# Performance work log

Hardware: AMD Instinct MI355X
Metric: run time of the kernel (lower is better)

## Reference

```python
import jax, jax.numpy as jnp
import numpy as np

N_NODES, N_EDGES, F_IN, HID, PROJ, N_CLS, N_GRAPHS, T_EMB = 50000, 800000, 128, 128, 512, 32, 256, 768
EPS_BN, EPS_LN = 1e-5, 1e-5


def setup_inputs() -> dict:
    key = jax.random.key(0)
    ks = jax.random.split(key, 24)
    s = 0.05
    inp = {
        "x": jax.random.normal(ks[0], (N_NODES, F_IN), jnp.float32),
        "edge_index": jax.random.randint(ks[1], (2, N_EDGES), 0, N_NODES),
        "batch": jnp.sort(jax.random.randint(ks[2], (N_NODES,), 0, N_GRAPHS)),
        "text_feats": jax.random.normal(ks[3], (N_GRAPHS, T_EMB), jnp.float32),
        # 4 stacked GCN layers (all 128->128), each with BatchNorm affine params
        "gcn_W": jax.random.normal(ks[4], (4, F_IN, HID), jnp.float32) * s,
        "gcn_b": jnp.zeros((4, HID), jnp.float32),
        "bn_g": jnp.ones((4, HID), jnp.float32),
        "bn_b": jnp.zeros((4, HID), jnp.float32),
        # graph projection head
        "gpj_W1": jax.random.normal(ks[5], (HID, PROJ), jnp.float32) * s,
        "gpj_b1": jnp.zeros((PROJ,), jnp.float32),
        "gpj_W2": jax.random.normal(ks[6], (PROJ, PROJ), jnp.float32) * s,
        "gpj_b2": jnp.zeros((PROJ,), jnp.float32),
        "gpj_g": jnp.ones((PROJ,), jnp.float32),
        "gpj_be": jnp.zeros((PROJ,), jnp.float32),
        "gcl_W": jax.random.normal(ks[7], (PROJ, N_CLS), jnp.float32) * s,
        "gcl_b": jnp.zeros((N_CLS,), jnp.float32),
        # text projection head
        "tpj_W1": jax.random.normal(ks[8], (T_EMB, PROJ), jnp.float32) * s,
        "tpj_b1": jnp.zeros((PROJ,), jnp.float32),
        "tpj_W2": jax.random.normal(ks[9], (PROJ, PROJ), jnp.float32) * s,
        "tpj_b2": jnp.zeros((PROJ,), jnp.float32),
        "tpj_g": jnp.ones((PROJ,), jnp.float32),
        "tpj_be": jnp.zeros((PROJ,), jnp.float32),
        "tcl_W": jax.random.normal(ks[10], (PROJ, N_CLS), jnp.float32) * s,
        "tcl_b": jnp.zeros((N_CLS,), jnp.float32),
    }
    return inp


def _gcn_layer(x, src, dst, dnorm, W, b):
    # PyG GCNConv with self-loops and symmetric normalization
    xw = x @ W  # [N, H]
    coef = dnorm[src] * dnorm[dst]  # [E]
    agg = jax.ops.segment_sum(xw[src] * coef[:, None], dst, num_segments=N_NODES)
    agg = agg + xw * (dnorm * dnorm)[:, None]  # self-loop contribution
    return agg + b


def _batch_norm(x, g, b):
    mu = jnp.mean(x, axis=0)
    var = jnp.mean((x - mu) ** 2, axis=0)
    return (x - mu) * jax.lax.rsqrt(var + EPS_BN) * g + b


def _projection_head(x, W1, b1, W2, b2, g, be):
    projected = x @ W1 + b1
    h = jax.nn.gelu(projected, approximate=False)
    h = h @ W2 + b2
    h = h + projected  # residual (dropout in eval mode = identity)
    mu = jnp.mean(h, axis=-1, keepdims=True)
    var = jnp.mean((h - mu) ** 2, axis=-1, keepdims=True)
    return (h - mu) * jax.lax.rsqrt(var + EPS_LN) * g + be


def reference(x, edge_index, batch, text_feats, gcn_W, gcn_b, bn_g, bn_b,
              gpj_W1, gpj_b1, gpj_W2, gpj_b2, gpj_g, gpj_be, gcl_W, gcl_b,
              tpj_W1, tpj_b1, tpj_W2, tpj_b2, tpj_g, tpj_be, tcl_W, tcl_b):
    src, dst = edge_index[0], edge_index[1]
    deg = jax.ops.segment_sum(jnp.ones((N_EDGES,), x.dtype), dst, num_segments=N_NODES) + 1.0
    dnorm = jax.lax.rsqrt(deg)
    h = x
    for i in range(4):  # input block, 2 hidden blocks, output block
        h = _gcn_layer(h, src, dst, dnorm, gcn_W[i], gcn_b[i])
        h = jax.nn.leaky_relu(h, negative_slope=0.01)
        h = _batch_norm(h, bn_g[i], bn_b[i])
    # global mean pool over graphs
    sums = jax.ops.segment_sum(h, batch, num_segments=N_GRAPHS)
    cnts = jax.ops.segment_sum(jnp.ones((N_NODES,), h.dtype), batch, num_segments=N_GRAPHS)
    g_emb = sums / jnp.maximum(cnts, 1.0)[:, None]  # [G, HID]

    graph_proj = _projection_head(g_emb, gpj_W1, gpj_b1, gpj_W2, gpj_b2, gpj_g, gpj_be)
    graph_logp = jax.nn.log_softmax(graph_proj @ gcl_W + gcl_b, axis=-1)

    text_proj = _projection_head(text_feats, tpj_W1, tpj_b1, tpj_W2, tpj_b2, tpj_g, tpj_be)
    text_logp = jax.nn.log_softmax(text_proj @ tcl_W + tcl_b, axis=-1)

    return (graph_proj, text_proj, graph_logp, text_logp)
```

## Files before the change

### kernel.cpp

```cpp
#include <hip/hip_runtime.h>
#include <hip/hip_bf16.h>

#define N_NODES 50000
#define N_EDGES 800000
#define F_IN    128
#define HID     128
#define PROJ    512
#define N_CLS   32
#define N_GRAPHS 256
#define T_EMB   768
#define NB_SCAN ((N_NODES + 255) / 256)
#define DBINS   1024
#define NBROW   ((N_NODES + 63) / 64)
#define NBG2    ((NBROW + 1) / 2)
#define SHW     6250
#define ESLICE  ((N_EDGES + 4095) / 4096)

typedef __attribute__((ext_vector_type(8))) short bf16x8;
typedef __attribute__((ext_vector_type(4))) float f32x4;

__device__ __forceinline__ float bf2f(unsigned short u) {
    unsigned v = ((unsigned)u) << 16;
    return __uint_as_float(v);
}
__device__ __forceinline__ unsigned short f2us(float v) {
    __hip_bfloat16 b = __float2bfloat16(v);
    union { __hip_bfloat16 b; unsigned short u; } c; c.b = b; return c.u;
}

__global__ __launch_bounds__(256) void k_deg(const int* __restrict__ ei,
                                             int* __restrict__ cnt, int nE) {
    int bx = blockIdx.x;
    int s = bx & 7;
    int slice = bx >> 3;
    int lo = s * SHW, hi = lo + SHW;
    int base = slice * 4096 + threadIdx.x;
#pragma unroll 4
    for (int u = 0; u < 16; u++) {
        int e = base + u * 256;
        if (e < nE) {
            int d = ei[nE + e];
            if (d >= lo && d < hi) atomicAdd(cnt + d, 1);
        }
    }
}

__global__ __launch_bounds__(256) void k_scan1(const int* __restrict__ cnt,
    int* __restrict__ rowstart, float* __restrict__ dnorm, int* __restrict__ bsum)
{
    __shared__ int ps[256];
    int t = threadIdx.x;
    int i = blockIdx.x * 256 + t;
    int c = (i < N_NODES) ? cnt[i] : 0;
    if (i < N_NODES) dnorm[i] = rsqrtf((float)c + 1.0f);
    ps[t] = c;
    __syncthreads();
    for (int off = 1; off < 256; off <<= 1) {
        int v = (t >= off) ? ps[t - off] : 0;
        __syncthreads();
        ps[t] += v;
        __syncthreads();
    }
    if (i < N_NODES) rowstart[i] = ps[t] - c;
    if (t == 255) bsum[blockIdx.x] = ps[255];
}

__global__ __launch_bounds__(256) void k_scan2(int* __restrict__ bsum) {
    __shared__ int ps[256];
    int t = threadIdx.x;
    int v = (t < NB_SCAN) ? bsum[t] : 0;
    ps[t] = v;
    __syncthreads();
    for (int off = 1; off < 256; off <<= 1) {
        int u = (t >= off) ? ps[t - off] : 0;
        __syncthreads();
        ps[t] += u;
        __syncthreads();
    }
    if (t < NB_SCAN) bsum[t] = ps[t] - v;
}

__global__ __launch_bounds__(256) void k_scan3(int* __restrict__ rowstart,
    const int* __restrict__ bsum, const int* __restrict__ cnt,
    int* __restrict__ dhist)
{
    __shared__ int lh[DBINS];
    int t = threadIdx.x;
    for (int k = t; k < DBINS; k += 256) lh[k] = 0;
    __syncthreads();
    int i = blockIdx.x * 256 + t;
    if (i < N_NODES) {
        rowstart[i] += bsum[blockIdx.x];
        atomicAdd(&lh[min(cnt[i], DBINS - 1)], 1);
    }
    if (i == 0) rowstart[N_NODES] = N_EDGES;
    __syncthreads();
    for (int k = t; k < DBINS; k += 256) {
        int v = lh[k];
        if (v) atomicAdd(dhist + k, v);
    }
}

__global__ __launch_bounds__(256) void k_dscan(const int* __restrict__ dhist,
                                               int* __restrict__ doff) {
    __shared__ int part[256];
    __shared__ int binv[DBINS];
    int t = threadIdx.x;
    int base = t * 4;
    int g0 = dhist[DBINS - 1 - (base + 0)];
    int g1 = dhist[DBINS - 1 - (base + 1)];
    int g2 = dhist[DBINS - 1 - (base + 2)];
    int g3 = dhist[DBINS - 1 - (base + 3)];
    int s = g0 + g1 + g2 + g3;
    part[t] = s;
    __syncthreads();
    for (int off = 1; off < 256; off <<= 1) {
        int v = (t >= off) ? part[t - off] : 0;
        __syncthreads();
        part[t] += v;
        __syncthreads();
    }
    int run = part[t] - s;
    binv[base + 0] = run; run += g0;
    binv[base + 1] = run; run += g1;
    binv[base + 2] = run; run += g2;
    binv[base + 3] = run; run += g3;
    __syncthreads();
    for (int k = t; k < DBINS; k += 256) doff[DBINS - 1 - k] = binv[k];
}

__global__ __launch_bounds__(1024) void k_dperm(const int* __restrict__ cnt,
    int* __restrict__ doff, int* __restrict__ rowperm)
{
    __shared__ int lh[DBINS];
    __shared__ int lbase[DBINS];
    int t = threadIdx.x;
    if (t < DBINS) lh[t] = 0;
    __syncthreads();
    int i = blockIdx.x * 1024 + t;
    int bin = 0, lrank = 0;
    bool ok = i < N_NODES;
    if (ok) {
        bin = min(cnt[i], DBINS - 1);
        lrank = atomicAdd(&lh[bin], 1);
    }
    __syncthreads();
    if (t < DBINS) {
        int v = lh[t];
        if (v) lbase[t] = atomicAdd(doff + t, v);
    }
    __syncthreads();
    if (ok) rowperm[lbase[bin] + lrank] = i;
}

__global__ __launch_bounds__(256) void k_fill(const int* __restrict__ ei,
    const int* __restrict__ rowstart, int* __restrict__ cursor,
    int* __restrict__ srcl, int nE)
{
    int bx = blockIdx.x;
    int s = bx & 7;
    int slice = bx >> 3;
    int lo = s * SHW, hi = lo + SHW;
    int base = slice * 4096 + threadIdx.x;
#pragma unroll 4
    for (int u = 0; u < 16; u++) {
        int e = base + u * 256;
        if (e < nE) {
            int d = ei[nE + e];
            if (d >= lo && d < hi) {
                int pos = rowstart[d] + atomicAdd(cursor + d, 1);
                srcl[pos] = ei[e];
            }
        }
    }
}

__global__ void k_prep(const float* __restrict__ W, unsigned short* __restrict__ Wt,
                       const int* __restrict__ batch, int* __restrict__ gstart) {
    int t = blockIdx.x * 256 + threadIdx.x;
    if (t < 4 * 128 * 128) {
        int l = t >> 14;
        int k = (t >> 7) & 127;
        int n = t & 127;
        Wt[(size_t)l * 16384 + n * 128 + k] = f2us(W[(size_t)l * 16384 + k * 128 + n]);
    } else {
        int r = t - 4 * 128 * 128;
        if (r <= N_NODES) {
            int b  = (r < N_NODES) ? batch[r] : N_GRAPHS;
            int bp = (r > 0) ? batch[r - 1] : -1;
            for (int g = bp + 1; g <= b && g <= N_GRAPHS; g++) gstart[g] = r;
        }
    }
}

__global__ __launch_bounds__(256) void k_gcn_mm_mfma(const void* __restrict__ inp,
    const unsigned short* __restrict__ Wt,
    const float* __restrict__ stats, const float* __restrict__ bng,
    const float* __restrict__ bnb, const float* __restrict__ dnorm,
    unsigned short* __restrict__ ph, int n)
{
    __shared__ __align__(16) unsigned short Bs[128][136];
    __shared__ float scs[128], shs[128];
    int t = threadIdx.x;
    int row0 = blockIdx.x * 64;

    if (stats && t < 128) {
        float inv_n = 1.0f / (float)N_NODES;
        float mu = stats[t] * inv_n;
        float var = stats[128 + t] * inv_n - mu * mu;
        float rs = rsqrtf(var + 1e-5f);
        float sc = rs * bng[t];
        scs[t] = sc;
        shs[t] = bnb[t] - mu * sc;
    }
#pragma unroll
    for (int i = 0; i < 8; i++) {
        int c = t + i * 256;
        int nn = c >> 4;
        int k8 = (c & 15) * 8;
        *(uint4*)&Bs[nn][k8] = *(const uint4*)(Wt + (size_t)nn * 128 + k8);
    }
    __syncthreads();

    int w = t >> 6, lane = t & 63;
    int m = lane & 15, quad = lane >> 4;
    int arow = row0 + w * 16 + m;
    bool rowok = arow < n;

    bf16x8 afrag[4];
    if (!stats) {
        const float* inf = (const float*)inp;
#pragma unroll
        for (int ki = 0; ki < 4; ki++) {
            int k8 = ki * 32 + quad * 8;
            float4 v0 = make_float4(0.f, 0.f, 0.f, 0.f);
            float4 v1 = make_float4(0.f, 0.f, 0.f, 0.f);
            if (rowok) {
                v0 = *(const float4*)(inf + (size_t)arow * 128 + k8);
                v1 = *(const float4*)(inf + (size_t)arow * 128 + k8 + 4);
            }
            union { unsigned short u[8]; bf16x8 v; } pk;
            pk.u[0] = f2us(v0.x); pk.u[1] = f2us(v0.y); pk.u[2] = f2us(v0.z); pk.u[3] = f2us(v0.w);
            pk.u[4] = f2us(v1.x); pk.u[5] = f2us(v1.y); pk.u[6] = f2us(v1.z); pk.u[7] = f2us(v1.w);
            afrag[ki] = pk.v;
        }
    } else {
        const unsigned short* inb = (const unsigned short*)inp;
#pragma unroll
        for (int ki = 0; ki < 4; ki++) {
            int k8 = ki * 32 + quad * 8;
            uint4 raw = make_uint4(0, 0, 0, 0);
            if (rowok) raw = *(const uint4*)(inb + (size_t)arow * 128 + k8);
            unsigned rr[4] = { raw.x, raw.y, raw.z, raw.w };
            union { unsigned short u[8]; bf16x8 v; } pk;
#pragma unroll
            for (int j = 0; j < 4; j++) {
                int f0 = k8 + 2 * j, f1 = k8 + 2 * j + 1;
                float a0 = bf2f((unsigned short)rr[j]) * scs[f0] + shs[f0];
                float a1 = bf2f((unsigned short)(rr[j] >> 16)) * scs[f1] + shs[f1];
                pk.u[2 * j] = f2us(a0);
                pk.u[2 * j + 1] = f2us(a1);
            }
            afrag[ki] = pk.v;
        }
    }

    f32x4 acc[8];
#pragma unroll
    for (int nt = 0; nt < 8; nt++) acc[nt] = (f32x4){0.f, 0.f, 0.f, 0.f};
#pragma unroll
    for (int ki = 0; ki < 4; ki++) {
#pragma unroll
        for (int nt = 0; nt < 8; nt++) {
            bf16x8 b = *(const bf16x8*)&Bs[nt * 16 + m][ki * 32 + quad * 8];
            acc[nt] = __builtin_amdgcn_mfma_f32_16x16x32_bf16(afrag[ki], b, acc[nt], 0, 0, 0);
        }
    }

    float dn[4];
#pragma unroll
    for (int reg = 0; reg < 4; reg++) {
        int gr = row0 + w * 16 + quad * 4 + reg;
        dn[reg] = (gr < n) ? dnorm[gr] : 0.f;
    }

    __syncthreads();
#pragma unroll
    for (int nt = 0; nt < 8; nt++) {
#pragma unroll
        for (int reg = 0; reg < 4; reg++) {
            Bs[w * 16 + quad * 4 + reg][nt * 16 + m] = f2us(acc[nt][reg] * dn[reg]);
        }
    }
    __syncthreads();
#pragma unroll
    for (int i = 0; i < 4; i++) {
        int idx = t + i * 256;
        int r = idx >> 4;
        int c8 = (idx & 15) * 8;
        int gr = row0 + r;
        int ch = c8 >> 5;
        int off = c8 & 31;
        if (gr < n)
            *(uint4*)(ph + (size_t)ch * (N_NODES * 32) + (size_t)gr * 32 + off)
                = *(const uint4*)&Bs[r][c8];
    }
}

__global__ __launch_bounds__(256) void k_gather_c(const uint4* __restrict__ ph128,
    const int* __restrict__ srcl, const int* __restrict__ rowstart,
    const int* __restrict__ rowperm, const float* __restrict__ dnorm,
    const float* __restrict__ bias, unsigned short* __restrict__ outbb,
    float* __restrict__ stats, int n)
{
    const int EMAX = N_EDGES - 1;
    __shared__ float bsm[32], bqm[32];
    int t = threadIdx.x;
    if (t < 32) { bsm[t] = 0.f; bqm[t] = 0.f; }
    __syncthreads();

    int bx = blockIdx.x;
    int xcd = bx & 7;
    int c = xcd >> 1;
    int rb = (bx >> 3) * 2 + (xcd & 1);
    if (rb >= NBROW) return;
    int lane = t & 63;
    int w = t >> 6;
    int grp = lane >> 2;
    int l4 = lane & 3;
    int idx = rb * 64 + w * 16 + grp;
    bool rok = idx < n;
    int r = rok ? rowperm[idx] : 0;
    int start = rowstart[r];
    int deg = rowstart[r + 1] - start;
    float dnr = dnorm[r];
    if (!rok) { deg = 0; dnr = 0.f; }
    int len = deg + 1;

    const uint4* phc = ph128 + (size_t)c * (N_NODES * 4);

    float bi[8];
#pragma unroll
    for (int k = 0; k < 8; k++) bi[k] = bias[c * 32 + l4 * 8 + k];

    float a[8];
#pragma unroll
    for (int k = 0; k < 8; k++) a[k] = 0.f;

    for (int j = 0; j < len; j += 4) {
        uint4 uv[4];
#pragma unroll
        for (int u = 0; u < 4; u++) {
            int i = j + u;
            int sl = srcl[min(start + i, EMAX)];
            int s = (i < deg) ? sl : r;
            uv[u] = phc[(size_t)s * 4 + l4];
        }
#pragma unroll
        for (int u = 0; u < 4; u++) {
            int i = j + u;
            float wt = (i < len) ? 1.f : 0.f;
            unsigned rr[4] = { uv[u].x, uv[u].y, uv[u].z, uv[u].w };
#pragma unroll
            for (int d = 0; d < 4; d++) {
                a[2 * d]     += wt * bf2f((unsigned short)rr[d]);
                a[2 * d + 1] += wt * bf2f((unsigned short)(rr[d] >> 16));
            }
        }
    }

    float v[8];
#pragma unroll
    for (int k = 0; k < 8; k++) {
        float x = a[k] * dnr + bi[k];
        v[k] = x > 0.f ? x : 0.01f * x;
    }
    if (rok) {
        union { unsigned short us[8]; uint4 u; } ov;
#pragma unroll
        for (int k = 0; k < 8; k++) ov.us[k] = f2us(v[k]);
        *(uint4*)(outbb + (size_t)r * 128 + c * 32 + l4 * 8) = ov.u;
    } else {
#pragma unroll
        for (int k = 0; k < 8; k++) v[k] = 0.f;
    }

    float q[8];
#pragma unroll
    for (int k = 0; k < 8; k++) q[k] = v[k] * v[k];
#pragma unroll
    for (int mk = 4; mk < 64; mk <<= 1) {
#pragma unroll
        for (int k = 0; k < 8; k++) {
            v[k] += __shfl_xor(v[k], mk, 64);
            q[k] += __shfl_xor(q[k], mk, 64);
        }
    }
    if (grp == 0) {
#pragma unroll
        for (int k = 0; k < 8; k++) {
            atomicAdd(&bsm[l4 * 8 + k], v[k]);
            atomicAdd(&bqm[l4 * 8 + k], q[k]);
        }
    }
    __syncthreads();
    if (t < 32) {
        atomicAdd(&stats[c * 32 + t], bsm[t]);
        atomicAdd(&stats[128 + c * 32 + t], bqm[t]);
    }
}

__global__ __launch_bounds__(256) void k_pool2(const unsigned short* __restrict__ outbb,
    const int* __restrict__ gstart, const float* __restrict__ stats,
    const float* __restrict__ bng, const float* __restrict__ bnb,
    float* __restrict__ gemb)
{
    __shared__ float scs[128], shs[128];
    int g = blockIdx.x;
    int t = threadIdx.x;
    if (t < 128) {
        float inv_n = 1.0f / (float)N_NODES;
        float mu = stats[t] * inv_n;
        float var = stats[128 + t] * inv_n - mu * mu;
        float rs = rsqrtf(var + 1e-5f);
        float sc = rs * bng[t];
        scs[t] = sc;
        shs[t] = bnb[t] - mu * sc;
    }
    __syncthreads();
    int f = t & 127;
    int half = t >> 7;
    int start = gstart[g], end = gstart[g + 1];
    int cnt = end - start;
    float s0 = 0.f, s1 = 0.f, s2 = 0.f, s3 = 0.f;
    int r = start + half;
    for (; r + 6 < end; r += 8) {
        s0 += bf2f(outbb[(size_t)(r    ) * 128 + f]);
        s1 += bf2f(outbb[(size_t)(r + 2) * 128 + f]);
        s2 += bf2f(outbb[(size_t)(r + 4) * 128 + f]);
        s3 += bf2f(outbb[(size_t)(r + 6) * 128 + f]);
    }
    for (; r < end; r += 2) s0 += bf2f(outbb[(size_t)r * 128 + f]);
    float sum = (s0 + s1) + (s2 + s3);
    __shared__ float sb[256];
    sb[t] = sum;
    __syncthreads();
    if (t < 128) {
        float tot = sb[t] + sb[t + 128];
        float v = (cnt > 0) ? (tot / (float)cnt) * scs[f] + shs[f] : 0.f;
        gemb[(size_t)g * 128 + f] = v;
    }
}

__global__ __launch_bounds__(256) void k_head1x(const float* __restrict__ gemb,
    const float* __restrict__ textf,
    const float* __restrict__ gW1, const float* __restrict__ tW1,
    float* __restrict__ projg, float* __restrict__ projt6)
{
    __shared__ float ins[8][128];
    int bx = blockIdx.x;
    int kc = blockIdx.z;
    int isT = bx >= 32;
    if (!isT && kc > 0) return;
    int rb = isT ? bx - 32 : bx;
    const float* in = isT ? textf : gemb;
    int K = isT ? T_EMB : HID;
    const float* W = isT ? tW1 : gW1;
    float* outp = isT ? (projt6 + (size_t)kc * (N_GRAPHS * PROJ)) : projg;
    int k0 = kc * 128;

    int t = threadIdx.x;
    {
        int r = t >> 5, k = (t & 31) * 4;
        *(float4*)&ins[r][k] = *(const float4*)(in + (size_t)(rb * 8 + r) * K + k0 + k);
    }
    __syncthreads();
    int col = blockIdx.y * 128 + (t & 127);
    int rg = t >> 7;
    float acc[4] = { 0.f, 0.f, 0.f, 0.f };
    const float* Wp = W + (size_t)k0 * 512 + col;
#pragma unroll 8
    for (int k = 0; k < 128; k++) {
        float w = Wp[(size_t)k * 512];
#pragma unroll
        for (int i = 0; i < 4; i++) acc[i] += ins[rg * 4 + i][k] * w;
    }
#pragma unroll
    for (int i = 0; i < 4; i++) {
        int row = rb * 8 + rg * 4 + i;
        outp[(size_t)row * 512 + col] = acc[i];
    }
}

__global__ __launch_bounds__(256) void k_head2c(
    const float* __restrict__ projg, const float* __restrict__ projt6,
    const float* __restrict__ gb1, const float* __restrict__ tb1,
    const float* __restrict__ gW2, const float* __restrict__ gb2,
    const float* __restrict__ gg, const float* __restrict__ gbe,
    const float* __restrict__ gclW, const float* __restrict__ gclb,
    const float* __restrict__ tW2, const float* __restrict__ tb2,
    const float* __restrict__ tg, const float* __restrict__ tbe,
    const float* __restrict__ tclW, const float* __restrict__ tclb,
    float* __restrict__ o_gproj, float* __restrict__ o_tproj,
    float* __restrict__ o_glogp, float* __restrict__ o_tlogp)
{
    __shared__ float prow[512], grow[512], onorm[512], red[256];
    __shared__ float part[8][32];
    __shared__ float logits[32];
    __shared__ float mred, lred;
    int bx = blockIdx.x;
    int isT = bx >= N_GRAPHS;
    int row = isT ? bx - N_GRAPHS : bx;
    const float* b1 = isT ? tb1 : gb1;
    const float* W2 = isT ? tW2 : gW2;
    const float* b2 = isT ? tb2 : gb2;
    const float* g  = isT ? tg  : gg;
    const float* be = isT ? tbe : gbe;
    const float* Wc = isT ? tclW : gclW;
    const float* bc = isT ? tclb : gclb;
    float* oproj = isT ? o_tproj : o_gproj;
    float* ologp = isT ? o_tlogp : o_glogp;

    int t = threadIdx.x;
    for (int c = t; c < 512; c += 256) {
        float p;
        if (isT) {
            const float* pp = projt6 + (size_t)row * 512 + c;
            p = pp[0];
#pragma unroll
            for (int s = 1; s < 6; s++) p += pp[(size_t)s * (N_GRAPHS * PROJ)];
        } else {
            p = projg[(size_t)row * 512 + c];
        }
        p += b1[c];
        prow[c] = p;
        grow[c] = 0.5f * p * (1.0f + erff(p * 0.70710678118f));
    }
    __syncthreads();
    float a0 = 0.f, a1 = 0.f;
    int c0 = t, c1 = t + 256;
    for (int k = 0; k < 512; k++) {
        float gk = grow[k];
        a0 += gk * W2[(size_t)k * 512 + c0];
        a1 += gk * W2[(size_t)k * 512 + c1];
    }
    float h0 = a0 + b2[c0] + prow[c0];
    float h1 = a1 + b2[c1] + prow[c1];
    red[t] = h0 + h1;
    __syncthreads();
    for (int s = 128; s > 0; s >>= 1) { if (t < s) red[t] += red[t + s]; __syncthreads(); }
    float mu = red[0] * (1.0f / 512.0f);
    __syncthreads();
    float d0 = h0 - mu, d1 = h1 - mu;
    red[t] = d0 * d0 + d1 * d1;
    __syncthreads();
    for (int s = 128; s > 0; s >>= 1) { if (t < s) red[t] += red[t + s]; __syncthreads(); }
    float rs = rsqrtf(red[0] * (1.0f / 512.0f) + 1e-5f);
    float o0 = d0 * rs * g[c0] + be[c0];
    float o1 = d1 * rs * g[c1] + be[c1];
    onorm[c0] = o0;
    onorm[c1] = o1;
    oproj[(size_t)row * 512 + c0] = o0;
    oproj[(size_t)row * 512 + c1] = o1;
    __syncthreads();

    int c = t & 31, seg = t >> 5;
    float p = 0.f;
    for (int k = seg * 64; k < seg * 64 + 64; k++)
        p += onorm[k] * Wc[(size_t)k * 32 + c];
    part[seg][c] = p;
    __syncthreads();
    if (t < 32) {
        float l = bc[t];
#pragma unroll
        for (int s = 0; s < 8; s++) l += part[s][t];
        logits[t] = l;
    }
    __syncthreads();
    if (t == 0) {
        float m = logits[0];
        for (int i = 1; i < 32; i++) m = fmaxf(m, logits[i]);
        float sum = 0.f;
        for (int i = 0; i < 32; i++) sum += expf(logits[i] - m);
        mred = m; lred = logf(sum);
    }
    __syncthreads();
    if (t < 32) ologp[(size_t)row * 32 + t] = logits[t] - mred - lred;
}

extern "C" void kernel_launch(void* const* d_in, const int* in_sizes, int n_in,
                              void* d_out, int out_size, void* d_ws, size_t ws_size,
                              hipStream_t stream) {
    const float* x     = (const float*)d_in[0];
    const int*   ei    = (const int*)d_in[1];
    const int*   batch = (const int*)d_in[2];
    const float* textf = (const float*)d_in[3];
    const float* gcnW  = (const float*)d_in[4];
    const float* gcnb  = (const float*)d_in[5];
    const float* bng   = (const float*)d_in[6];
    const float* bnb   = (const float*)d_in[7];
    const float* gW1   = (const float*)d_in[8];
    const float* gb1   = (const float*)d_in[9];
    const float* gW2   = (const float*)d_in[10];
    const float* gb2   = (const float*)d_in[11];
    const float* gg    = (const float*)d_in[12];
    const float* gbe   = (const float*)d_in[13];
    const float* gclW  = (const float*)d_in[14];
    const float* gclb  = (const float*)d_in[15];
    const float* tW1   = (const float*)d_in[16];
    const float* tb1   = (const float*)d_in[17];
    const float* tW2   = (const float*)d_in[18];
    const float* tb2   = (const float*)d_in[19];
    const float* tg    = (const float*)d_in[20];
    const float* tbe   = (const float*)d_in[21];
    const float* tclW  = (const float*)d_in[22];
    const float* tclb  = (const float*)d_in[23];

    const int N = N_NODES, E = N_EDGES;
    const int NF = N * HID;

    float* p = (float*)d_ws;
    unsigned short* outbb = (unsigned short*)p; p += NF / 2;
    unsigned short* ph    = (unsigned short*)p; p += NF / 2;
    unsigned short* Wt    = (unsigned short*)p; p += 4 * 16384 / 2;
    float* dnorm  = p; p += N;
    float* gemb   = p; p += N_GRAPHS * HID;
    float* projg  = p; p += N_GRAPHS * PROJ;
    float* projt6 = p; p += 6 * N_GRAPHS * PROJ;
    int* cnt      = (int*)p; p += N;
    int* cursor   = (int*)p; p += N;
    float* stats4 = p; p += 4 * 256;
    int* dhist    = (int*)p; p += DBINS;
    int* rowstart = (int*)p; p += N + 1;
    int* gstart   = (int*)p; p += N_GRAPHS + 1;
    int* bsum     = (int*)p; p += 256;
    int* srcl     = (int*)p; p += E;
    int* doff     = (int*)p; p += DBINS;
    int* rowperm  = (int*)p; p += N;

    float* outp = (float*)d_out;
    float* o_gproj = outp;
    float* o_tproj = outp + N_GRAPHS * PROJ;
    float* o_glogp = o_tproj + N_GRAPHS * PROJ;
    float* o_tlogp = o_glogp + N_GRAPHS * N_CLS;

    hipMemsetAsync(cnt, 0, (size_t)(2 * N + 4 * 256 + DBINS) * sizeof(int), stream);
    k_deg<<<ESLICE * 8, 256, 0, stream>>>(ei, cnt, E);
    k_scan1<<<NB_SCAN, 256, 0, stream>>>(cnt, rowstart, dnorm, bsum);
    k_scan2<<<1, 256, 0, stream>>>(bsum);
    k_scan3<<<NB_SCAN, 256, 0, stream>>>(rowstart, bsum, cnt, dhist);
    k_fill<<<ESLICE * 8, 256, 0, stream>>>(ei, rowstart, cursor, srcl, E);
    k_dscan<<<1, 256, 0, stream>>>(dhist, doff);
    k_dperm<<<(N + 1023) / 1024, 1024, 0, stream>>>(cnt, doff, rowperm);
    k_prep<<<(4 * 16384 + N + 1 + 255) / 256, 256, 0, stream>>>(gcnW, Wt, batch, gstart);

    for (int l = 0; l < 4; l++) {
        const void* in = (l == 0) ? (const void*)x : (const void*)outbb;
        const float* st = (l == 0) ? nullptr : stats4 + (l - 1) * 256;
        const float* bg = (l == 0) ? nullptr : bng + (size_t)(l - 1) * HID;
        const float* bb = (l == 0) ? nullptr : bnb + (size_t)(l - 1) * HID;
        k_gcn_mm_mfma<<<(N + 63) / 64, 256, 0, stream>>>(in, Wt + (size_t)l * 16384,
                                                         st, bg, bb, dnorm, ph, N);
        k_gather_c<<<NBG2 * 8, 256, 0, stream>>>((const uint4*)ph, srcl,
                                                 rowstart, rowperm, dnorm,
                                                 gcnb + (size_t)l * HID, outbb,
                                                 stats4 + l * 256, N);
    }

    k_pool2<<<N_GRAPHS, 256, 0, stream>>>(outbb, gstart, stats4 + 3 * 256,
                                          bng + 3 * HID, bnb + 3 * HID, gemb);

    k_head1x<<<dim3(64, 4, 6), 256, 0, stream>>>(gemb, textf, gW1, tW1, projg, projt6);
    k_head2c<<<2 * N_GRAPHS, 256, 0, stream>>>(projg, projt6, gb1, tb1,
                                               gW2, gb2, gg, gbe, gclW, gclb,
                                               tW2, tb2, tg, tbe, tclW, tclb,
                                               o_gproj, o_tproj, o_glogp, o_tlogp);
}
```

Before: 462.9 us.

## Split projection head second GEMM into tiled split-K kernel with prep and epilogue

Replaces the single per-row head kernel, which read the full 512x512 W2 matrix once for every output row, with three kernels. A prep kernel adds the bias and applies GELU, a tiled split-K GEMM shares each W2 load across 8 rows, and an epilogue sums the partials before layernorm and log-softmax. This cuts the redundant weight traffic and exposes more parallelism, at the cost of two extra launches and partial-sum round trips through global memory.

```diff
diff --git a/kernel.cpp b/kernel.cpp
--- a/kernel.cpp
+++ b/kernel.cpp
@@ -492,27 +492,92 @@
     }
 }
 
-__global__ __launch_bounds__(256) void k_head2c(
-    const float* __restrict__ projg, const float* __restrict__ projt6,
-    const float* __restrict__ gb1, const float* __restrict__ tb1,
-    const float* __restrict__ gW2, const float* __restrict__ gb2,
-    const float* __restrict__ gg, const float* __restrict__ gbe,
-    const float* __restrict__ gclW, const float* __restrict__ gclb,
-    const float* __restrict__ tW2, const float* __restrict__ tb2,
-    const float* __restrict__ tg, const float* __restrict__ tbe,
-    const float* __restrict__ tclW, const float* __restrict__ tclb,
+__global__ __launch_bounds__(256) void k_hprep(const float* __restrict__ projg,
+    const float* __restrict__ projt6, const float* __restrict__ gb1,
+    const float* __restrict__ tb1, float* __restrict__ prow_buf,
+    float* __restrict__ grow_buf)
+{
+    int idx = (blockIdx.x * 256 + threadIdx.x) * 4;
+    int row = idx >> 9;
+    int c = idx & 511;
+    int isT = row >= N_GRAPHS;
+    int lrow = row & (N_GRAPHS - 1);
+    const float* b1 = isT ? tb1 : gb1;
+    float4 p;
+    if (isT) {
+        const float* pp = projt6 + (size_t)lrow * 512 + c;
+        p = *(const float4*)pp;
+#pragma unroll
+        for (int s = 1; s < 6; s++) {
+            float4 q = *(const float4*)(pp + (size_t)s * (N_GRAPHS * PROJ));
+            p.x += q.x; p.y += q.y; p.z += q.z; p.w += q.w;
+        }
+    } else {
+        p = *(const float4*)(projg + (size_t)lrow * 512 + c);
+    }
+    float4 b = *(const float4*)(b1 + c);
+    p.x += b.x; p.y += b.y; p.z += b.z; p.w += b.w;
+    *(float4*)(prow_buf + (size_t)row * 512 + c) = p;
+    float4 g;
+    g.x = 0.5f * p.x * (1.0f + erff(p.x * 0.70710678118f));
+    g.y = 0.5f * p.y * (1.0f + erff(p.y * 0.70710678118f));
+    g.z = 0.5f * p.z * (1.0f + erff(p.z * 0.70710678118f));
+    g.w = 0.5f * p.w * (1.0f + erff(p.w * 0.70710678118f));
+    *(float4*)(grow_buf + (size_t)row * 512 + c) = g;
+}
+
+__global__ __launch_bounds__(256) void k_head2a(const float* __restrict__ grow_buf,
+    const float* __restrict__ gW2, const float* __restrict__ tW2,
+    float* __restrict__ h2p)
+{
+    __shared__ float gs[8][128];
+    int rb = blockIdx.x;
+    int cc = blockIdx.y;
+    int kc = blockIdx.z;
+    int isT = rb >= 32;
+    const float* W2 = isT ? tW2 : gW2;
+    int t = threadIdx.x;
+    {
+        int r = t >> 5, k4 = (t & 31) * 4;
+        *(float4*)&gs[r][k4] =
+            *(const float4*)(grow_buf + (size_t)(rb * 8 + r) * 512 + kc * 128 + k4);
+    }
+    __syncthreads();
+    int col = cc * 128 + (t & 127);
+    int rg = t >> 7;
+    float acc[4] = { 0.f, 0.f, 0.f, 0.f };
+    const float* Wp = W2 + (size_t)(kc * 128) * 512 + col;
+#pragma unroll 8
+    for (int k = 0; k < 128; k++) {
+        float w = Wp[(size_t)k * 512];
+#pragma unroll
+        for (int i = 0; i < 4; i++) acc[i] += gs[rg * 4 + i][k] * w;
+    }
+#pragma unroll
+    for (int i = 0; i < 4; i++) {
+        int row = rb * 8 + rg * 4 + i;
+        h2p[(size_t)kc * (512 * 512) + (size_t)row * 512 + col] = acc[i];
+    }
+}
+
+__global__ __launch_bounds__(256) void k_head2b(const float* __restrict__ h2p,
+    const float* __restrict__ prow_buf,
+    const float* __restrict__ gb2, const float* __restrict__ gg,
+    const float* __restrict__ gbe, const float* __restrict__ gclW,
+    const float* __restrict__ gclb,
+    const float* __restrict__ tb2, const float* __restrict__ tg,
+    const float* __restrict__ tbe, const float* __restrict__ tclW,
+    const float* __restrict__ tclb,
     float* __restrict__ o_gproj, float* __restrict__ o_tproj,
     float* __restrict__ o_glogp, float* __restrict__ o_tlogp)
 {
-    __shared__ float prow[512], grow[512], onorm[512], red[256];
+    __shared__ float onorm[512], red[256];
     __shared__ float part[8][32];
     __shared__ float logits[32];
     __shared__ float mred, lred;
     int bx = blockIdx.x;
     int isT = bx >= N_GRAPHS;
-    int row = isT ? bx - N_GRAPHS : bx;
-    const float* b1 = isT ? tb1 : gb1;
-    const float* W2 = isT ? tW2 : gW2;
+    int row = bx & (N_GRAPHS - 1);
     const float* b2 = isT ? tb2 : gb2;
     const float* g  = isT ? tg  : gg;
     const float* be = isT ? tbe : gbe;
@@ -522,30 +587,15 @@
     float* ologp = isT ? o_tlogp : o_glogp;
 
     int t = threadIdx.x;
-    for (int c = t; c < 512; c += 256) {
-        float p;
-        if (isT) {
-            const float* pp = projt6 + (size_t)row * 512 + c;
-            p = pp[0];
-#pragma unroll
-            for (int s = 1; s < 6; s++) p += pp[(size_t)s * (N_GRAPHS * PROJ)];
-        } else {
-            p = projg[(size_t)row * 512 + c];
-        }
-        p += b1[c];
-        prow[c] = p;
-        grow[c] = 0.5f * p * (1.0f + erff(p * 0.70710678118f));
-    }
-    __syncthreads();
-    float a0 = 0.f, a1 = 0.f;
     int c0 = t, c1 = t + 256;
-    for (int k = 0; k < 512; k++) {
-        float gk = grow[k];
-        a0 += gk * W2[(size_t)k * 512 + c0];
-        a1 += gk * W2[(size_t)k * 512 + c1];
-    }
-    float h0 = a0 + b2[c0] + prow[c0];
-    float h1 = a1 + b2[c1] + prow[c1];
+    size_t base = (size_t)bx * 512;
+    float h0 = prow_buf[base + c0] + b2[c0];
+    float h1 = prow_buf[base + c1] + b2[c1];
+#pragma unroll
+    for (int kc = 0; kc < 4; kc++) {
+        h0 += h2p[(size_t)kc * (512 * 512) + base + c0];
+        h1 += h2p[(size_t)kc * (512 * 512) + base + c1];
+    }
     red[t] = h0 + h1;
     __syncthreads();
     for (int s = 128; s > 0; s >>= 1) { if (t < s) red[t] += red[t + s]; __syncthreads(); }
@@ -623,10 +673,13 @@
     unsigned short* outbb = (unsigned short*)p; p += NF / 2;
     unsigned short* ph    = (unsigned short*)p; p += NF / 2;
     unsigned short* Wt    = (unsigned short*)p; p += 4 * 16384 / 2;
-    float* dnorm  = p; p += N;
-    float* gemb   = p; p += N_GRAPHS * HID;
-    float* projg  = p; p += N_GRAPHS * PROJ;
-    float* projt6 = p; p += 6 * N_GRAPHS * PROJ;
+    float* dnorm    = p; p += N;
+    float* gemb     = p; p += N_GRAPHS * HID;
+    float* projg    = p; p += N_GRAPHS * PROJ;
+    float* projt6   = p; p += 6 * N_GRAPHS * PROJ;
+    float* prow_buf = p; p += 512 * PROJ;
+    float* grow_buf = p; p += 512 * PROJ;
+    float* h2p      = p; p += 4 * 512 * PROJ;
     int* cnt      = (int*)p; p += N;
     int* cursor   = (int*)p; p += N;
     float* stats4 = p; p += 4 * 256;
@@ -671,8 +724,10 @@
                                           bng + 3 * HID, bnb + 3 * HID, gemb);
 
     k_head1x<<<dim3(64, 4, 6), 256, 0, stream>>>(gemb, textf, gW1, tW1, projg, projt6);
-    k_head2c<<<2 * N_GRAPHS, 256, 0, stream>>>(projg, projt6, gb1, tb1,
-                                               gW2, gb2, gg, gbe, gclW, gclb,
-                                               tW2, tb2, tg, tbe, tclW, tclb,
-                                               o_gproj, o_tproj, o_glogp, o_tlogp);
-}
+    k_hprep<<<256, 256, 0, stream>>>(projg, projt6, gb1, tb1, prow_buf, grow_buf);
+    k_head2a<<<dim3(64, 4, 4), 256, 0, stream>>>(grow_buf, gW2, tW2, h2p);
+    k_head2b<<<512, 256, 0, stream>>>(h2p, prow_buf,
+                                      gb2, gg, gbe, gclW, gclb,
+                                      tb2, tg, tbe, tclW, tclb,
+                                      o_gproj, o_tproj, o_glogp, o_tlogp);
+}
```

Result: no change. 457.7 us (-1.1%).
